# Optimization experiments

Measured on AMD Instinct MI355X. Metric: run time of the kernel, lower is better.

## Reference

```python
import jax, jax.numpy as jnp
import numpy as np

VOCAB = 1_000_000
EMBED_DIM = 64
BATCH = 16384
NUM_FEATS = 50


def setup_inputs() -> dict:
    key = jax.random.key(0)
    k_idx, k_tab = jax.random.split(key)
    indices = jax.random.randint(k_idx, (BATCH, NUM_FEATS), 0, VOCAB, dtype=jnp.int64 if jax.config.jax_enable_x64 else jnp.int32)
    # Learned table standing in for the warm (all-hit) HierarchicalKV hash table.
    init_std = np.sqrt(2.0 / EMBED_DIM).astype(np.float32)
    table = jax.random.normal(k_tab, (VOCAB, EMBED_DIM), dtype=jnp.float32) * init_std
    return {"indices": indices, "table": table}


def reference(indices, table):
    # forward: flatten, find_or_insert (== gather in the all-hit path), reshape back
    # indices: [B, F] int, table: [V, D] -> out: [B, F, D]
    flat = indices.reshape(-1)
    emb = jnp.take(table, flat, axis=0)  # [B*F, D] memory-bound gather
    return emb.reshape(*indices.shape, table.shape[-1])
```

## Files before the change

### kernel.cpp

```cpp
#include <hip/hip_runtime.h>


#define LANES_PER_ROW 16

typedef float floatx4 __attribute__((ext_vector_type(4)));

__global__ __launch_bounds__(256) void hh_embed_gather(
    const int* __restrict__ idx,
    const floatx4* __restrict__ table,
    floatx4* __restrict__ out,
    int n_rows, int quarter_rows)
{
    int tid  = blockIdx.x * blockDim.x + threadIdx.x;
    int row0 = tid >> 4;
    int lane = tid & 15;
    if (row0 >= quarter_rows) return;
    int row1 = row0 + quarter_rows;
    int row2 = row1 + quarter_rows;
    int row3 = row2 + quarter_rows;
    bool has1 = (row1 < n_rows);
    bool has2 = (row2 < n_rows);
    bool has3 = (row3 < n_rows);

    int t0 = idx[row0];
    int t1 = has1 ? idx[row1] : 0;
    int t2 = has2 ? idx[row2] : 0;
    int t3 = has3 ? idx[row3] : 0;

    floatx4 v0 = table[(long long)t0 * LANES_PER_ROW + lane];
    floatx4 v1 = table[(long long)t1 * LANES_PER_ROW + lane];
    floatx4 v2 = table[(long long)t2 * LANES_PER_ROW + lane];
    floatx4 v3 = table[(long long)t3 * LANES_PER_ROW + lane];

    __builtin_nontemporal_store(v0, out + (long long)row0 * LANES_PER_ROW + lane);
    if (has1) __builtin_nontemporal_store(v1, out + (long long)row1 * LANES_PER_ROW + lane);
    if (has2) __builtin_nontemporal_store(v2, out + (long long)row2 * LANES_PER_ROW + lane);
    if (has3) __builtin_nontemporal_store(v3, out + (long long)row3 * LANES_PER_ROW + lane);
}

extern "C" void kernel_launch(void* const* d_in, const int* in_sizes, int n_in,
                              void* d_out, int out_size, void* d_ws, size_t ws_size,
                              hipStream_t stream) {
    const int*   idx   = (const int*)d_in[0];
    const float* table = (const float*)d_in[1];
    float*       out   = (float*)d_out;

    int n_rows = in_sizes[0];
    int quarter_rows = (n_rows + 3) / 4;
    long long total_threads = (long long)quarter_rows * LANES_PER_ROW;
    int block = 256;
    int grid  = (int)((total_threads + block - 1) / block);

    hh_embed_gather<<<grid, block, 0, stream>>>(
        idx, (const floatx4*)table, (floatx4*)out, n_rows, quarter_rows);
}
```

Measured before the change: 396.7 us.

## Bucketize lookups by table region before gathering embedding rows

Adds a pre-pass that sorts the (row, index) pairs into 16 buckets by the high bits of the table index, using shared and global atomics. A second kernel then gathers table rows bucket by bucket, so that concurrent lookups touch a narrower slice of the table and DRAM/cache locality improves. The cost is an extra memset, an extra kernel launch, atomic traffic, a workspace round trip for the pairs, and a grid sized for full bucket capacity in which many threads exit early. Rows are silently dropped if any bucket overflows its fixed capacity. The fallback kernel also loses its four-rows-per-thread unrolling.

```diff
diff --git a/kernel.cpp b/kernel.cpp
--- a/kernel.cpp
+++ b/kernel.cpp
@@ -1,41 +1,70 @@
 #include <hip/hip_runtime.h>
 
 
+typedef float floatx4 __attribute__((ext_vector_type(4)));
+
 #define LANES_PER_ROW 16
+#define NBUCKET 16
+#define BUCKET_SHIFT 16
+#define BUCKET_CAP 65536
 
-typedef float floatx4 __attribute__((ext_vector_type(4)));
+__global__ __launch_bounds__(256) void bucketize(
+    const int* __restrict__ idx, int n_rows,
+    int* __restrict__ gcnt, int2* __restrict__ pairs)
+{
+    __shared__ int cnt[NBUCKET];
+    __shared__ int base[NBUCKET];
+    int tid = threadIdx.x;
+    if (tid < NBUCKET) cnt[tid] = 0;
+    __syncthreads();
+
+    int row = blockIdx.x * 256 + tid;
+    bool valid = (row < n_rows);
+    int t = 0, b = 0, pos = 0;
+    if (valid) {
+        t = idx[row];
+        b = t >> BUCKET_SHIFT;
+        pos = atomicAdd(&cnt[b], 1);
+    }
+    __syncthreads();
+    if (tid < NBUCKET)
+        base[tid] = atomicAdd(&gcnt[tid], cnt[tid]);
+    __syncthreads();
+    if (valid) {
+        int p = base[b] + pos;
+        if (p < BUCKET_CAP)
+            pairs[b * BUCKET_CAP + p] = make_int2(row, t);
+    }
+}
+
+__global__ __launch_bounds__(256) void gather_bucketed(
+    const int* __restrict__ gcnt, const int2* __restrict__ pairs,
+    const floatx4* __restrict__ table, floatx4* __restrict__ out)
+{
+    int gid   = blockIdx.x * 256 + threadIdx.x;
+    int entry = gid >> 4;
+    int lane  = gid & 15;
+    int b     = entry >> 16;
+    int slot  = entry & (BUCKET_CAP - 1);
+    if (slot >= gcnt[b]) return;
+    int2 pr = pairs[entry];
+    floatx4 v = table[(long long)pr.y * LANES_PER_ROW + lane];
+    __builtin_nontemporal_store(v, out + (long long)pr.x * LANES_PER_ROW + lane);
+}
 
 __global__ __launch_bounds__(256) void hh_embed_gather(
     const int* __restrict__ idx,
     const floatx4* __restrict__ table,
     floatx4* __restrict__ out,
-    int n_rows, int quarter_rows)
+    int n_rows)
 {
     int tid  = blockIdx.x * blockDim.x + threadIdx.x;
-    int row0 = tid >> 4;
+    int row  = tid >> 4;
     int lane = tid & 15;
-    if (row0 >= quarter_rows) return;
-    int row1 = row0 + quarter_rows;
-    int row2 = row1 + quarter_rows;
-    int row3 = row2 + quarter_rows;
-    bool has1 = (row1 < n_rows);
-    bool has2 = (row2 < n_rows);
-    bool has3 = (row3 < n_rows);
-
-    int t0 = idx[row0];
-    int t1 = has1 ? idx[row1] : 0;
-    int t2 = has2 ? idx[row2] : 0;
-    int t3 = has3 ? idx[row3] : 0;
-
-    floatx4 v0 = table[(long long)t0 * LANES_PER_ROW + lane];
-    floatx4 v1 = table[(long long)t1 * LANES_PER_ROW + lane];
-    floatx4 v2 = table[(long long)t2 * LANES_PER_ROW + lane];
-    floatx4 v3 = table[(long long)t3 * LANES_PER_ROW + lane];
-
-    __builtin_nontemporal_store(v0, out + (long long)row0 * LANES_PER_ROW + lane);
-    if (has1) __builtin_nontemporal_store(v1, out + (long long)row1 * LANES_PER_ROW + lane);
-    if (has2) __builtin_nontemporal_store(v2, out + (long long)row2 * LANES_PER_ROW + lane);
-    if (has3) __builtin_nontemporal_store(v3, out + (long long)row3 * LANES_PER_ROW + lane);
+    if (row >= n_rows) return;
+    int t = idx[row];
+    floatx4 v = table[(long long)t * LANES_PER_ROW + lane];
+    __builtin_nontemporal_store(v, out + (long long)row * LANES_PER_ROW + lane);
 }
 
 extern "C" void kernel_launch(void* const* d_in, const int* in_sizes, int n_in,
@@ -44,13 +73,28 @@
     const int*   idx   = (const int*)d_in[0];
     const float* table = (const float*)d_in[1];
     float*       out   = (float*)d_out;
+    int n_rows = in_sizes[0];
 
-    int n_rows = in_sizes[0];
-    int quarter_rows = (n_rows + 3) / 4;
-    long long total_threads = (long long)quarter_rows * LANES_PER_ROW;
-    int block = 256;
-    int grid  = (int)((total_threads + block - 1) / block);
+    size_t need = 256 + (size_t)NBUCKET * BUCKET_CAP * sizeof(int2);
+    bool can_bucket = (ws_size >= need) && (n_rows <= NBUCKET * BUCKET_CAP);
 
-    hh_embed_gather<<<grid, block, 0, stream>>>(
-        idx, (const floatx4*)table, (floatx4*)out, n_rows, quarter_rows);
+    if (can_bucket) {
+        int*  gcnt  = (int*)d_ws;
+        int2* pairs = (int2*)((char*)d_ws + 256);
+
+        hipMemsetAsync(d_ws, 0, 256, stream);
+
+        int gridA = (n_rows + 255) / 256;
+        bucketize<<<gridA, 256, 0, stream>>>(idx, n_rows, gcnt, pairs);
+
+        long long slots = (long long)NBUCKET * BUCKET_CAP;
+        int gridB = (int)(slots * LANES_PER_ROW / 256);
+        gather_bucketed<<<gridB, 256, 0, stream>>>(
+            gcnt, pairs, (const floatx4*)table, (floatx4*)out);
+    } else {
+        long long total_threads = (long long)n_rows * LANES_PER_ROW;
+        int grid = (int)((total_threads + 255) / 256);
+        hh_embed_gather<<<grid, 256, 0, stream>>>(
+            idx, (const floatx4*)table, (floatx4*)out, n_rows);
+    }
 }
```

Result: slower. 437.6 us (+10.3%).
